# Kernel optimization log

Measured on AMD Instinct MI355X. Metric: run time of the kernel, lower is better.

## Reference

```python
import jax, jax.numpy as jnp
import numpy as np

NUM_SENT, SENT_LEN, HIDDEN, OUT = 128, 64, 512, 512
N = NUM_SENT * SENT_LEN


def setup_inputs() -> dict:
    key = jax.random.key(0)
    ks = jax.random.split(key, 14)
    s = 1.0 / np.sqrt(HIDDEN)
    so = 1.0 / np.sqrt(OUT)
    return {
        "x": jax.random.normal(ks[0], (NUM_SENT, SENT_LEN, HIDDEN), jnp.float32),
        "mask": jax.random.uniform(ks[1], (N,), jnp.float32),
        "a_ud": jax.random.normal(ks[2], (N, N), jnp.float32) * 0.01,
        "a_lr": jax.random.normal(ks[3], (N, N), jnp.float32) * 0.01,
        "W": jax.random.uniform(ks[4], (OUT, HIDDEN), jnp.float32, -s, s),
        "b": jax.random.uniform(ks[5], (OUT,), jnp.float32, -s, s),
        "W_ud": jax.random.uniform(ks[6], (OUT, HIDDEN), jnp.float32, -s, s),
        "b_ud": jax.random.uniform(ks[7], (OUT,), jnp.float32, -s, s),
        "W_lr": jax.random.uniform(ks[8], (OUT, HIDDEN), jnp.float32, -s, s),
        "b_lr": jax.random.uniform(ks[9], (OUT,), jnp.float32, -s, s),
        "W_g": jax.random.uniform(ks[10], (OUT, HIDDEN), jnp.float32, -s, s),
        "b_g": jax.random.uniform(ks[11], (OUT,), jnp.float32, -s, s),
        "W_go": jax.random.uniform(ks[12], (OUT, OUT), jnp.float32, -so, so),
        "b_go": jax.random.uniform(ks[13], (OUT,), jnp.float32, -so, so),
    }


def reference(x, mask, a_ud, a_lr, W, b, W_ud, b_ud, W_lr, b_lr, W_g, b_g, W_go, b_go):
    num_sent, sent_len, hidden = x.shape
    xf = x.reshape(-1, hidden)                       # [N, H]
    h_ud = a_ud @ xf                                 # [N, H] neighbor aggregation (up/down)
    h_lr = a_lr @ xf                                 # [N, H] neighbor aggregation (left/right)
    h = (xf @ W.T + b) + (h_ud @ W_ud.T + b_ud) + (h_lr @ W_lr.T + b_lr)  # [N, OUT]
    # global node branch: masked mean-pool of relu(linear_g(x))
    n = mask.sum()
    h_g = (mask[None, :] @ jax.nn.relu(xf @ W_g.T + b_g)) / n  # [1, OUT]
    h = h + (h_g @ W_go.T + b_go)                    # broadcast add over N rows
    h = jax.nn.relu(h).reshape(num_sent, sent_len, -1)
    return (h, h_g)
```

## Files before the change

kernel.cpp:

```cpp
#include <hip/hip_runtime.h>
#include <stdint.h>


typedef __attribute__((ext_vector_type(8))) short short8;
typedef __attribute__((ext_vector_type(4))) float f32x4;

typedef const __attribute__((address_space(1))) void* gas1_t;
typedef __attribute__((address_space(3))) void* las3_t;

__device__ __forceinline__ void gload16(const void* g, void* l) {
  __builtin_amdgcn_global_load_lds((gas1_t)g, (las3_t)l, 16, 0, 0);
}

__device__ __forceinline__ unsigned pack2t(float lo, float hi) {
  return __builtin_amdgcn_perm(__float_as_uint(hi), __float_as_uint(lo), 0x07060302u);
}

__device__ __forceinline__ unsigned f2bf_rne(float f) {
  unsigned u = __float_as_uint(f);
  return (u + 0x7FFFu + ((u >> 16) & 1u)) >> 16;
}
__device__ __forceinline__ unsigned pack2_rne(float lo, float hi) {
  return f2bf_rne(lo) | (f2bf_rne(hi) << 16);
}

__global__ __launch_bounds__(256) void k1_convert(
    const float* __restrict__ x, const float* __restrict__ W,
    const float* __restrict__ W_ud, const float* __restrict__ W_lr,
    const float* __restrict__ W_g,
    uint16_t* __restrict__ xb, uint16_t* __restrict__ Yt, uint16_t* __restrict__ Wb1)
{
  unsigned tid = blockIdx.x * 256u + threadIdx.x;
  const float* src;
  uint16_t* dst;
  if (tid < 524288u) {
    src = x + (size_t)tid * 8;
    dst = xb + (size_t)tid * 8;
  } else {
    unsigned r = tid - 524288u;
    unsigned which = r >> 15;
    unsigned e8 = (r & 32767u) * 8;
    src = (which == 0 ? W : which == 1 ? W_ud : which == 2 ? W_lr : W_g) + e8;
    if (which == 0) {
      unsigned n = e8 >> 9, k = e8 & 511u;
      dst = Yt + (size_t)n * 16896 + 16384 + k;
    } else {
      dst = Wb1 + (size_t)(which - 1) * 262144 + e8;
    }
  }
  float4 v0 = ((const float4*)src)[0];
  float4 v1 = ((const float4*)src)[1];
  uint4 p;
  p.x = pack2_rne(v0.x, v0.y); p.y = pack2_rne(v0.z, v0.w);
  p.z = pack2_rne(v1.x, v1.y); p.w = pack2_rne(v1.z, v1.w);
  *(uint4*)dst = p;
}

__global__ __launch_bounds__(256) void k2_gemm1(
    const uint16_t* __restrict__ xb, const uint16_t* __restrict__ Wb1,
    const float* __restrict__ mask, const float* __restrict__ b_g,
    uint16_t* __restrict__ Yt, float* __restrict__ colsum)
{
  __shared__ __align__(16) char smem[34816];
  char* const A0 = smem;
  char* const B0 = smem + 8192;
  char* const A1 = smem + 16384;
  char* const B1 = smem + 24576;

  const int t = threadIdx.x;
  const int i0 = blockIdx.x * 128;
  const int bn = blockIdx.y;
  const int n0 = bn * 128;
  const int lane = t & 63, w = t >> 6;
  const int q = lane >> 4, l15 = lane & 15;
  const int wm = w >> 1, wn = w & 1;
  const int srow = t >> 2;
  const int sw = (t & 3) ^ ((srow >> 1) & 3);

  f32x4 acc[4][4] = {};

  const uint16_t* const aA0 = xb + (size_t)(i0 + srow) * 512 + sw * 8;
  const uint16_t* const aA1 = aA0 + (size_t)64 * 512;
  const uint16_t* const aB0 = Wb1 + (size_t)(n0 + srow) * 512 + sw * 8;
  const uint16_t* const aB1 = aB0 + (size_t)64 * 512;

  gload16(aA0, A0 + t * 16);
  gload16(aA1, A0 + 4096 + t * 16);
  gload16(aB0, B0 + t * 16);
  gload16(aB1, B0 + 4096 + t * 16);

  for (int s = 0; s < 16; ++s) {
    __syncthreads();
    if (s < 15) {
      const int kk = (s + 1) << 5;
      char* const nA = (s & 1) ? A0 : A1;
      char* const nB = (s & 1) ? B0 : B1;
      gload16(aA0 + kk, nA + t * 16);
      gload16(aA1 + kk, nA + 4096 + t * 16);
      gload16(aB0 + kk, nB + t * 16);
      gload16(aB1 + kk, nB + 4096 + t * 16);
    }
    char* const cA = (s & 1) ? A1 : A0;
    char* const cB = (s & 1) ? B1 : B0;
    short8 af[4], bf[4];
#pragma unroll
    for (int mi = 0; mi < 4; ++mi) {
      const int r = wm * 64 + mi * 16 + l15;
      af[mi] = *(const short8*)(cA + r * 64 + ((q ^ ((r >> 1) & 3)) * 16));
    }
#pragma unroll
    for (int ni = 0; ni < 4; ++ni) {
      const int r = wn * 64 + ni * 16 + l15;
      bf[ni] = *(const short8*)(cB + r * 64 + ((q ^ ((r >> 1) & 3)) * 16));
    }
#pragma unroll
    for (int mi = 0; mi < 4; ++mi)
#pragma unroll
      for (int ni = 0; ni < 4; ++ni)
        acc[mi][ni] = __builtin_amdgcn_mfma_f32_16x16x32_bf16(af[mi], bf[ni], acc[mi][ni], 0, 0, 0);
  }
  __syncthreads();

  const int g = bn >> 2;
  const int jb = (bn & 3) * 128;

  if (g < 2) {
    uint16_t* T = (uint16_t*)smem;
#pragma unroll
    for (int mi = 0; mi < 4; ++mi) {
#pragma unroll
      for (int ni = 0; ni < 4; ++ni) {
        int jl = wn * 64 + ni * 16 + l15;
#pragma unroll
        for (int r = 0; r < 4; ++r) {
          int il = wm * 64 + mi * 16 + q * 4 + r;
          T[jl * 136 + il] = (uint16_t)f2bf_rne(acc[mi][ni][r]);
        }
      }
    }
    __syncthreads();
    const int jl = t >> 1, half = t & 1;
    uint16_t* dst = Yt + (size_t)(jb + jl) * 16896 + (size_t)g * 8192 + i0 + half * 64;
    const uint16_t* srcT = T + jl * 136 + half * 64;
#pragma unroll
    for (int c = 0; c < 8; ++c)
      *(uint4*)(dst + c * 8) = *(const uint4*)(srcT + c * 8);
  } else {
    float mk[4][4];
#pragma unroll
    for (int mi = 0; mi < 4; ++mi)
#pragma unroll
      for (int r = 0; r < 4; ++r)
        mk[mi][r] = mask[i0 + wm * 64 + mi * 16 + q * 4 + r];
#pragma unroll
    for (int ni = 0; ni < 4; ++ni) {
      const int jl = jb + wn * 64 + ni * 16 + l15;
      const float bg = b_g[jl];
      float p = 0.f;
#pragma unroll
      for (int mi = 0; mi < 4; ++mi)
#pragma unroll
        for (int r = 0; r < 4; ++r)
          p += fmaxf(acc[mi][ni][r] + bg, 0.f) * mk[mi][r];
      p += __shfl_xor(p, 16);
      p += __shfl_xor(p, 32);
      if (q == 0) atomicAdd(&colsum[jl], p);
    }
  }
}

__global__ __launch_bounds__(256) void k4_finalize(
    const float* __restrict__ colsum, const float* __restrict__ mask,
    const float* __restrict__ b, const float* __restrict__ b_ud,
    const float* __restrict__ b_lr, const float* __restrict__ W_go,
    const float* __restrict__ b_go,
    float* __restrict__ row_add, float* __restrict__ out_hg)
{
  __shared__ float red[256];
  __shared__ float hg[512];
  const int t = threadIdx.x;
  float s = 0.f;
  for (int k = t; k < 8192; k += 256) s += mask[k];
  red[t] = s;
  __syncthreads();
  for (int o = 128; o > 0; o >>= 1) {
    if (t < o) red[t] += red[t + o];
    __syncthreads();
  }
  const float n = red[0];
  for (int j = t; j < 512; j += 256) hg[j] = colsum[j] / n;
  __syncthreads();

  const int j0 = blockIdx.x * 64;
  const int jj = j0 + (t >> 2);
  const int seg = t & 3;
  const float4* wrow = (const float4*)(W_go + (size_t)jj * 512 + seg * 128);
  float p = 0.f;
#pragma unroll 4
  for (int c = 0; c < 32; ++c) {
    float4 wv = wrow[c];
    const float* h4 = &hg[seg * 128 + c * 4];
    p += wv.x * h4[0] + wv.y * h4[1] + wv.z * h4[2] + wv.w * h4[3];
  }
  p += __shfl_down(p, 2);
  p += __shfl_down(p, 1);
  if ((t & 3) == 0)
    row_add[jj] = b[jj] + b_ud[jj] + b_lr[jj] + b_go[jj] + p;
  if (t < 64) out_hg[j0 + t] = hg[j0 + t];
}

__global__ __launch_bounds__(256, 3) void k5_gemm_big(
    const float* __restrict__ a_ud, const float* __restrict__ a_lr,
    const float* __restrict__ x, const uint16_t* __restrict__ Yt,
    float* __restrict__ out, float* __restrict__ P, int nsteps)
{
  __shared__ __align__(16) char smem[34816];
  char* const A0 = smem;
  char* const A1 = smem + 9216;
  char* const B0 = smem + 18432;
  char* const B1 = smem + 26624;

  const int t = threadIdx.x;
  const int i0 = blockIdx.x * 128;
  const int j0 = blockIdx.y * 128;
  const int z  = blockIdx.z;
  const int lane = t & 63;
  const int q = lane >> 4, l15 = lane & 15;
  const int w = t >> 6;
  const int wm = w >> 1, wn = w & 1;

  const int arow = t >> 1, ahalf = t & 1;
  const int brow = t >> 2;
  const int bchunk = (t & 3) ^ ((t >> 3) & 3);

  f32x4 acc[4][4] = {};
  const int kbase0 = z * (nsteps << 5);

  float4 aX0, aX1, aX2, aX3, aY0, aY1, aY2, aY3;

#define A_SRC(gk) ((gk) < 8192 \
    ? a_ud + (size_t)(i0 + arow) * 8192 + (gk) + ahalf * 16 \
    : ((gk) < 16384 \
      ? a_lr + (size_t)(i0 + arow) * 8192 + ((gk) - 8192) + ahalf * 16 \
      : x + (size_t)(i0 + arow) * 512 + ((gk) - 16384) + ahalf * 16))

#define LOAD_A(R0, R1, R2, R3, gk) { \
    const float* as_ = A_SRC(gk); \
    R0 = ((const float4*)as_)[0]; R1 = ((const float4*)as_)[1]; \
    R2 = ((const float4*)as_)[2]; R3 = ((const float4*)as_)[3]; }

#define LOAD_B(dstB, gk) { \
    gload16(Yt + (size_t)(j0 + brow) * 16896 + (gk) + bchunk * 8, (dstB) + t * 16); \
    gload16(Yt + (size_t)(j0 + brow + 64) * 16896 + (gk) + bchunk * 8, (dstB) + 4096 + t * 16); }

#define PACK_A(dstA, R0, R1, R2, R3) { \
    uint4 p0_, p1_; \
    p0_.x = pack2t(R0.x, R0.y); p0_.y = pack2t(R0.z, R0.w); \
    p0_.z = pack2t(R1.x, R1.y); p0_.w = pack2t(R1.z, R1.w); \
    p1_.x = pack2t(R2.x, R2.y); p1_.y = pack2t(R2.z, R2.w); \
    p1_.z = pack2t(R3.x, R3.y); p1_.w = pack2t(R3.z, R3.w); \
    *(uint4*)((dstA) + arow * 72 + ahalf * 32) = p0_; \
    *(uint4*)((dstA) + arow * 72 + ahalf * 32 + 16) = p1_; }

  LOAD_A(aX0, aX1, aX2, aX3, kbase0);
  __builtin_amdgcn_sched_barrier(0);
  LOAD_B(B0, kbase0);
  __builtin_amdgcn_sched_barrier(0);
  LOAD_A(aY0, aY1, aY2, aY3, kbase0 + 32);
  __builtin_amdgcn_sched_barrier(0);
  PACK_A(A0, aX0, aX1, aX2, aX3);
  asm volatile("s_waitcnt vmcnt(4) lgkmcnt(0)" ::: "memory");
  __builtin_amdgcn_sched_barrier(0);
  __builtin_amdgcn_s_barrier();
  __builtin_amdgcn_sched_barrier(0);

#define K5_BODY(s_, LX0, LX1, LX2, LX3, PX0, PX1, PX2, PX3) { \
    const int s__ = (s_); \
    char* const cA_ = (s__ & 1) ? A1 : A0; \
    char* const cB_ = (s__ & 1) ? B1 : B0; \
    char* const nA_ = (s__ & 1) ? A0 : A1; \
    char* const nB_ = (s__ & 1) ? B0 : B1; \
    const bool h1_ = (s__ + 1 < nsteps); \
    const bool h2_ = (s__ + 2 < nsteps); \
    if (h1_) { LOAD_B(nB_, kbase0 + ((s__ + 1) << 5)); } \
    __builtin_amdgcn_sched_barrier(0); \
    if (h2_) { LOAD_A(LX0, LX1, LX2, LX3, kbase0 + ((s__ + 2) << 5)); } \
    __builtin_amdgcn_sched_barrier(0); \
    short8 af_[4], bf_[4]; \
    _Pragma("unroll") \
    for (int mi_ = 0; mi_ < 4; ++mi_) \
      af_[mi_] = *(const short8*)(cA_ + (wm * 64 + mi_ * 16 + l15) * 72 + q * 16); \
    _Pragma("unroll") \
    for (int ni_ = 0; ni_ < 4; ++ni_) { \
      const int j_ = wn * 64 + ni_ * 16 + l15; \
      bf_[ni_] = *(const short8*)(cB_ + j_ * 64 + ((q ^ ((j_ >> 1) & 3)) * 16)); \
    } \
    _Pragma("unroll") \
    for (int mi_ = 0; mi_ < 4; ++mi_) \
      _Pragma("unroll") \
      for (int ni_ = 0; ni_ < 4; ++ni_) \
        acc[mi_][ni_] = __builtin_amdgcn_mfma_f32_16x16x32_bf16(af_[mi_], bf_[ni_], acc[mi_][ni_], 0, 0, 0); \
    if (h1_) { PACK_A(nA_, PX0, PX1, PX2, PX3); } \
    if (h2_) { asm volatile("s_waitcnt vmcnt(4) lgkmcnt(0)" ::: "memory"); } \
    else     { asm volatile("s_waitcnt vmcnt(0) lgkmcnt(0)" ::: "memory"); } \
    __builtin_amdgcn_sched_barrier(0); \
    __builtin_amdgcn_s_barrier(); \
    __builtin_amdgcn_sched_barrier(0); \
  }

  for (int s = 0; s < nsteps; s += 2) {
    K5_BODY(s,     aX0, aX1, aX2, aX3, aY0, aY1, aY2, aY3);
    K5_BODY(s + 1, aY0, aY1, aY2, aY3, aX0, aX1, aX2, aX3);
  }
#undef K5_BODY
#undef PACK_A
#undef LOAD_B
#undef LOAD_A
#undef A_SRC

  float* dst = z ? P + (size_t)(z - 1) * 4194304 : out;
#pragma unroll
  for (int ni = 0; ni < 4; ++ni) {
    const int jl = j0 + wn * 64 + ni * 16 + l15;
#pragma unroll
    for (int mi = 0; mi < 4; ++mi)
#pragma unroll
      for (int r = 0; r < 4; ++r) {
        const int il = i0 + wm * 64 + mi * 16 + q * 4 + r;
        dst[(size_t)il * 512 + jl] = acc[mi][ni][r];
      }
  }
}

__global__ __launch_bounds__(256) void k6_combine(
    const float* __restrict__ P, const float* __restrict__ row_add,
    float* __restrict__ out, int npart)
{
  const int idx = blockIdx.x * 256 + threadIdx.x;
  float4 a = ((const float4*)out)[idx];
  for (int p = 0; p < npart; ++p) {
    const float4 v = ((const float4*)P)[(size_t)p * 1048576 + idx];
    a.x += v.x; a.y += v.y; a.z += v.z; a.w += v.w;
  }
  const float4 r = ((const float4*)row_add)[idx & 127];
  float4 o;
  o.x = fmaxf(a.x + r.x, 0.f);
  o.y = fmaxf(a.y + r.y, 0.f);
  o.z = fmaxf(a.z + r.z, 0.f);
  o.w = fmaxf(a.w + r.w, 0.f);
  ((float4*)out)[idx] = o;
}

extern "C" void kernel_launch(void* const* d_in, const int* in_sizes, int n_in,
                              void* d_out, int out_size, void* d_ws, size_t ws_size,
                              hipStream_t stream) {
  (void)in_sizes; (void)n_in; (void)out_size;
  const float* x    = (const float*)d_in[0];
  const float* mask = (const float*)d_in[1];
  const float* a_ud = (const float*)d_in[2];
  const float* a_lr = (const float*)d_in[3];
  const float* W    = (const float*)d_in[4];
  const float* b    = (const float*)d_in[5];
  const float* W_ud = (const float*)d_in[6];
  const float* b_ud = (const float*)d_in[7];
  const float* W_lr = (const float*)d_in[8];
  const float* b_lr = (const float*)d_in[9];
  const float* W_g  = (const float*)d_in[10];
  const float* b_g  = (const float*)d_in[11];
  const float* W_go = (const float*)d_in[12];
  const float* b_go = (const float*)d_in[13];
  float* out = (float*)d_out;

  char* ws = (char*)d_ws;
  uint16_t* xb     = (uint16_t*)(ws);
  uint16_t* Yt     = (uint16_t*)(ws + 8388608);
  uint16_t* Wb1    = (uint16_t*)(ws + 25690112);
  float*    colsum = (float*)(ws + 27262976);
  float*    rowadd = (float*)(ws + 27265024);
  float*    P      = (float*)(ws + 27267072);

  const int Z = (ws_size >= 77598720u) ? 4 : 2;
  const int nsteps = (16896 / Z) / 32;

  hipMemsetAsync(colsum, 0, 512 * sizeof(float), stream);
  k1_convert<<<2560, 256, 0, stream>>>(x, W, W_ud, W_lr, W_g, xb, Yt, Wb1);
  k2_gemm1<<<dim3(64, 12), 256, 0, stream>>>(xb, Wb1, mask, b_g, Yt, colsum);
  k4_finalize<<<8, 256, 0, stream>>>(colsum, mask, b, b_ud, b_lr, W_go, b_go,
                                     rowadd, out + 4194304);
  k5_gemm_big<<<dim3(64, 4, Z), 256, 0, stream>>>(a_ud, a_lr, x, Yt, out, P, nsteps);
  k6_combine<<<4096, 256, 0, stream>>>(P, rowadd, out, Z - 1);
}
```

Baseline: 931.6 us.

## Drop LDS staging in big GEMM and load MFMA operands directly into registers

Rewrites the main split-K GEMM to skip shared memory. Each wave loads its A fragments (fp32, packed to bf16 in registers) and B fragments straight from global memory, with register double-buffering. The output tile shrinks from 128x128 to 128x64, the grid doubles in y and occupancy is raised to 4. This removes LDS writes, reads and barriers, but A data is no longer shared across the wn waves. The A matrix, which dominates traffic, is therefore read twice as often from global/L2, and the strided per-lane loads are less coalesced.

```diff
diff --git a/kernel.cpp b/kernel.cpp
--- a/kernel.cpp
+++ b/kernel.cpp
@@ -209,119 +209,86 @@
   if (t < 64) out_hg[j0 + t] = hg[j0 + t];
 }
 
-__global__ __launch_bounds__(256, 3) void k5_gemm_big(
+__global__ __launch_bounds__(256, 4) void k5_gemm_big(
     const float* __restrict__ a_ud, const float* __restrict__ a_lr,
     const float* __restrict__ x, const uint16_t* __restrict__ Yt,
     float* __restrict__ out, float* __restrict__ P, int nsteps)
 {
-  __shared__ __align__(16) char smem[34816];
-  char* const A0 = smem;
-  char* const A1 = smem + 9216;
-  char* const B0 = smem + 18432;
-  char* const B1 = smem + 26624;
-
   const int t = threadIdx.x;
   const int i0 = blockIdx.x * 128;
-  const int j0 = blockIdx.y * 128;
+  const int j0 = blockIdx.y * 64;
   const int z  = blockIdx.z;
   const int lane = t & 63;
   const int q = lane >> 4, l15 = lane & 15;
   const int w = t >> 6;
   const int wm = w >> 1, wn = w & 1;
 
-  const int arow = t >> 1, ahalf = t & 1;
-  const int brow = t >> 2;
-  const int bchunk = (t & 3) ^ ((t >> 3) & 3);
-
-  f32x4 acc[4][4] = {};
+  f32x4 acc[4][2] = {};
   const int kbase0 = z * (nsteps << 5);
-
-  float4 aX0, aX1, aX2, aX3, aY0, aY1, aY2, aY3;
-
-#define A_SRC(gk) ((gk) < 8192 \
-    ? a_ud + (size_t)(i0 + arow) * 8192 + (gk) + ahalf * 16 \
-    : ((gk) < 16384 \
-      ? a_lr + (size_t)(i0 + arow) * 8192 + ((gk) - 8192) + ahalf * 16 \
-      : x + (size_t)(i0 + arow) * 512 + ((gk) - 16384) + ahalf * 16))
-
-#define LOAD_A(R0, R1, R2, R3, gk) { \
-    const float* as_ = A_SRC(gk); \
-    R0 = ((const float4*)as_)[0]; R1 = ((const float4*)as_)[1]; \
-    R2 = ((const float4*)as_)[2]; R3 = ((const float4*)as_)[3]; }
-
-#define LOAD_B(dstB, gk) { \
-    gload16(Yt + (size_t)(j0 + brow) * 16896 + (gk) + bchunk * 8, (dstB) + t * 16); \
-    gload16(Yt + (size_t)(j0 + brow + 64) * 16896 + (gk) + bchunk * 8, (dstB) + 4096 + t * 16); }
-
-#define PACK_A(dstA, R0, R1, R2, R3) { \
-    uint4 p0_, p1_; \
-    p0_.x = pack2t(R0.x, R0.y); p0_.y = pack2t(R0.z, R0.w); \
-    p0_.z = pack2t(R1.x, R1.y); p0_.w = pack2t(R1.z, R1.w); \
-    p1_.x = pack2t(R2.x, R2.y); p1_.y = pack2t(R2.z, R2.w); \
-    p1_.z = pack2t(R3.x, R3.y); p1_.w = pack2t(R3.z, R3.w); \
-    *(uint4*)((dstA) + arow * 72 + ahalf * 32) = p0_; \
-    *(uint4*)((dstA) + arow * 72 + ahalf * 32 + 16) = p1_; }
-
-  LOAD_A(aX0, aX1, aX2, aX3, kbase0);
-  __builtin_amdgcn_sched_barrier(0);
-  LOAD_B(B0, kbase0);
-  __builtin_amdgcn_sched_barrier(0);
-  LOAD_A(aY0, aY1, aY2, aY3, kbase0 + 32);
-  __builtin_amdgcn_sched_barrier(0);
-  PACK_A(A0, aX0, aX1, aX2, aX3);
-  asm volatile("s_waitcnt vmcnt(4) lgkmcnt(0)" ::: "memory");
-  __builtin_amdgcn_sched_barrier(0);
-  __builtin_amdgcn_s_barrier();
-  __builtin_amdgcn_sched_barrier(0);
-
-#define K5_BODY(s_, LX0, LX1, LX2, LX3, PX0, PX1, PX2, PX3) { \
-    const int s__ = (s_); \
-    char* const cA_ = (s__ & 1) ? A1 : A0; \
-    char* const cB_ = (s__ & 1) ? B1 : B0; \
-    char* const nA_ = (s__ & 1) ? A0 : A1; \
-    char* const nB_ = (s__ & 1) ? B0 : B1; \
-    const bool h1_ = (s__ + 1 < nsteps); \
-    const bool h2_ = (s__ + 2 < nsteps); \
-    if (h1_) { LOAD_B(nB_, kbase0 + ((s__ + 1) << 5)); } \
-    __builtin_amdgcn_sched_barrier(0); \
-    if (h2_) { LOAD_A(LX0, LX1, LX2, LX3, kbase0 + ((s__ + 2) << 5)); } \
-    __builtin_amdgcn_sched_barrier(0); \
-    short8 af_[4], bf_[4]; \
+  const int arow0 = i0 + wm * 64 + l15;
+
+  float4 aX[4][2], aY[4][2];
+  short8 bX[2], bY[2];
+
+#define LOAD_A_SET(dst, gk_) { \
+    const int gk5_ = (gk_); \
+    const float* base5_; int ld5_; int kk5_; \
+    if (gk5_ < 8192)       { base5_ = a_ud; ld5_ = 8192; kk5_ = gk5_; } \
+    else if (gk5_ < 16384) { base5_ = a_lr; ld5_ = 8192; kk5_ = gk5_ - 8192; } \
+    else                   { base5_ = x;    ld5_ = 512;  kk5_ = gk5_ - 16384; } \
+    const float* ap5_ = base5_ + (size_t)arow0 * ld5_ + kk5_ + q * 8; \
     _Pragma("unroll") \
-    for (int mi_ = 0; mi_ < 4; ++mi_) \
-      af_[mi_] = *(const short8*)(cA_ + (wm * 64 + mi_ * 16 + l15) * 72 + q * 16); \
+    for (int mi_ = 0; mi_ < 4; ++mi_) { \
+      const float* r5_ = ap5_ + (size_t)(mi_ * 16) * ld5_; \
+      dst[mi_][0] = ((const float4*)r5_)[0]; \
+      dst[mi_][1] = ((const float4*)r5_)[1]; \
+    } }
+
+#define LOAD_B_SET(dst, gk_) { \
     _Pragma("unroll") \
-    for (int ni_ = 0; ni_ < 4; ++ni_) { \
-      const int j_ = wn * 64 + ni_ * 16 + l15; \
-      bf_[ni_] = *(const short8*)(cB_ + j_ * 64 + ((q ^ ((j_ >> 1) & 3)) * 16)); \
-    } \
+    for (int ni_ = 0; ni_ < 2; ++ni_) { \
+      const uint16_t* bp5_ = Yt + (size_t)(j0 + wn * 32 + ni_ * 16 + l15) * 16896 \
+                              + (gk_) + q * 8; \
+      dst[ni_] = *(const short8*)bp5_; \
+    } }
+
+#define K5_BODY(av, bv) { \
     _Pragma("unroll") \
-    for (int mi_ = 0; mi_ < 4; ++mi_) \
-      _Pragma("unroll") \
-      for (int ni_ = 0; ni_ < 4; ++ni_) \
-        acc[mi_][ni_] = __builtin_amdgcn_mfma_f32_16x16x32_bf16(af_[mi_], bf_[ni_], acc[mi_][ni_], 0, 0, 0); \
-    if (h1_) { PACK_A(nA_, PX0, PX1, PX2, PX3); } \
-    if (h2_) { asm volatile("s_waitcnt vmcnt(4) lgkmcnt(0)" ::: "memory"); } \
-    else     { asm volatile("s_waitcnt vmcnt(0) lgkmcnt(0)" ::: "memory"); } \
-    __builtin_amdgcn_sched_barrier(0); \
-    __builtin_amdgcn_s_barrier(); \
-    __builtin_amdgcn_sched_barrier(0); \
-  }
-
-  for (int s = 0; s < nsteps; s += 2) {
-    K5_BODY(s,     aX0, aX1, aX2, aX3, aY0, aY1, aY2, aY3);
-    K5_BODY(s + 1, aY0, aY1, aY2, aY3, aX0, aX1, aX2, aX3);
-  }
+    for (int mi_ = 0; mi_ < 4; ++mi_) { \
+      uint4 u5_; \
+      u5_.x = pack2t(av[mi_][0].x, av[mi_][0].y); \
+      u5_.y = pack2t(av[mi_][0].z, av[mi_][0].w); \
+      u5_.z = pack2t(av[mi_][1].x, av[mi_][1].y); \
+      u5_.w = pack2t(av[mi_][1].z, av[mi_][1].w); \
+      short8 af5_ = *(short8*)&u5_; \
+      acc[mi_][0] = __builtin_amdgcn_mfma_f32_16x16x32_bf16(af5_, bv[0], acc[mi_][0], 0, 0, 0); \
+      acc[mi_][1] = __builtin_amdgcn_mfma_f32_16x16x32_bf16(af5_, bv[1], acc[mi_][1], 0, 0, 0); \
+    } }
+
+  LOAD_A_SET(aX, kbase0);
+  LOAD_B_SET(bX, kbase0);
+  LOAD_A_SET(aY, kbase0 + 32);
+  LOAD_B_SET(bY, kbase0 + 32);
+
+  for (int s = 0; s < nsteps - 2; s += 2) {
+    K5_BODY(aX, bX);
+    LOAD_A_SET(aX, kbase0 + ((s + 2) << 5));
+    LOAD_B_SET(bX, kbase0 + ((s + 2) << 5));
+    K5_BODY(aY, bY);
+    LOAD_A_SET(aY, kbase0 + ((s + 3) << 5));
+    LOAD_B_SET(bY, kbase0 + ((s + 3) << 5));
+  }
+  K5_BODY(aX, bX);
+  K5_BODY(aY, bY);
+
 #undef K5_BODY
-#undef PACK_A
-#undef LOAD_B
-#undef LOAD_A
-#undef A_SRC
+#undef LOAD_B_SET
+#undef LOAD_A_SET
 
   float* dst = z ? P + (size_t)(z - 1) * 4194304 : out;
 #pragma unroll
-  for (int ni = 0; ni < 4; ++ni) {
-    const int jl = j0 + wn * 64 + ni * 16 + l15;
+  for (int ni = 0; ni < 2; ++ni) {
+    const int jl = j0 + wn * 32 + ni * 16 + l15;
 #pragma unroll
     for (int mi = 0; mi < 4; ++mi)
 #pragma unroll
@@ -387,6 +354,6 @@
   k2_gemm1<<<dim3(64, 12), 256, 0, stream>>>(xb, Wb1, mask, b_g, Yt, colsum);
   k4_finalize<<<8, 256, 0, stream>>>(colsum, mask, b, b_ud, b_lr, W_go, b_go,
                                      rowadd, out + 4194304);
-  k5_gemm_big<<<dim3(64, 4, Z), 256, 0, stream>>>(a_ud, a_lr, x, Yt, out, P, nsteps);
+  k5_gemm_big<<<dim3(64, 8, Z), 256, 0, stream>>>(a_ud, a_lr, x, Yt, out, P, nsteps);
   k6_combine<<<4096, 256, 0, stream>>>(P, rowadd, out, Z - 1);
 }
```

Result: slower. 1.622 ms (+74.1%).
